# Performance work log

Hardware: AMD Instinct MI355X
Metric: run time of the kernel (lower is better)

The kernel has to match this reference:

```python
import jax, jax.numpy as jnp
import numpy as np

V, E, H, NLAB, NL = 30000, 512, 256, 20, 2
B, T = 32, 512


def setup_inputs() -> dict:
    key = jax.random.key(0)
    ks = jax.random.split(key, 11)
    s = 0.05
    return {
        "input": jax.random.randint(ks[0], (B, T), 0, V, dtype=jnp.int32),
        "mask": jnp.ones((B, T), dtype=bool),
        "embed_table": jax.random.normal(ks[1], (V, E), jnp.float32) * s,
        "Wih": jax.random.normal(ks[2], (NL, 2, 4 * H, E), jnp.float32) * s,  # layer input dim E == 2H
        "Whh": jax.random.normal(ks[3], (NL, 2, 4 * H, H), jnp.float32) * s,
        "bias": jax.random.normal(ks[4], (NL, 2, 4 * H), jnp.float32) * s,  # b_ih + b_hh fused
        "lin_W": jax.random.normal(ks[5], (NLAB, 2 * H), jnp.float32) * s,
        "lin_b": jax.random.normal(ks[6], (NLAB,), jnp.float32) * s,
        "transitions": jax.random.normal(ks[7], (NLAB, NLAB), jnp.float32) * 0.1,
        "start_trans": jax.random.normal(ks[8], (NLAB,), jnp.float32) * 0.1,
        "end_trans": jax.random.normal(ks[9], (NLAB,), jnp.float32) * 0.1,
    }


def _lstm_dir(x, Wih, Whh, b, reverse):
    # x: [B,T,in] -> hs: [B,T,H]
    pre = jnp.swapaxes(x, 0, 1) @ Wih.T + b  # [T,B,4H] input projection precomputed
    h0 = jnp.zeros((x.shape[0], Whh.shape[1]), x.dtype)

    def step(carry, p):
        h, c = carry
        g = p + h @ Whh.T
        i, f, gg, o = jnp.split(g, 4, axis=-1)  # pytorch gate order i,f,g,o
        i = jax.nn.sigmoid(i); f = jax.nn.sigmoid(f)
        gg = jnp.tanh(gg); o = jax.nn.sigmoid(o)
        c = f * c + i * gg
        h = o * jnp.tanh(c)
        return (h, c), h

    _, hs = jax.lax.scan(step, (h0, h0), pre, reverse=reverse)
    return jnp.swapaxes(hs, 0, 1)


def _bilstm(x, Wih, Whh, bias):
    out = x
    for l in range(Wih.shape[0]):
        f = _lstm_dir(out, Wih[l, 0], Whh[l, 0], bias[l, 0], False)
        bwd = _lstm_dir(out, Wih[l, 1], Whh[l, 1], bias[l, 1], True)
        out = jnp.concatenate([f, bwd], axis=-1)
    return out


def _viterbi(em, mask, trans, start, end):
    # em: [B,T,L], mask: [B,T] (mask[:,0] assumed all True, as torchcrf requires)
    Bz, Tz, Lz = em.shape
    ar = jnp.arange(Lz, dtype=jnp.int32)
    score0 = start[None, :] + em[:, 0]

    def step(score, xs):
        em_t, m_t = xs  # [B,L], [B]
        ns = score[:, :, None] + trans[None] + em_t[:, None, :]  # [B,L_prev,L_cur]
        best = ns.max(axis=1)
        idx = ns.argmax(axis=1).astype(jnp.int32)
        score = jnp.where(m_t[:, None], best, score)
        idx = jnp.where(m_t[:, None], idx, ar[None, :])  # identity bp for padded steps
        return score, idx

    em_tb = jnp.swapaxes(em, 0, 1)
    m_tb = jnp.swapaxes(mask, 0, 1)
    score, hist = jax.lax.scan(step, score0, (em_tb[1:], m_tb[1:]))
    score = score + end[None, :]
    last = jnp.argmax(score, axis=-1).astype(jnp.int32)
    bidx = jnp.arange(Bz)

    def back(tag, bp):
        prev = bp[bidx, tag]
        return prev, prev

    _, prevs = jax.lax.scan(back, last, hist, reverse=True)  # prevs[t] = tag_t for t=0..T-2
    tags = jnp.concatenate([prevs, last[None]], axis=0)  # [T,B]
    return jnp.swapaxes(tags, 0, 1), score.max(axis=-1)


def reference(input, mask, embed_table, Wih, Whh, bias, lin_W, lin_b, transitions, start_trans, end_trans):
    x = embed_table[input]                      # [B,T,E]
    h = _bilstm(x, Wih, Whh, bias)              # [B,T,2H]
    em = h @ lin_W.T + lin_b                    # [B,T,L]
    tags, _ = _viterbi(em, mask, transitions, start_trans, end_trans)
    return tags
```

## Files before the change

kernel.cpp:

```cpp
#include <hip/hip_runtime.h>
#include <math.h>


#define T_SEQ   512
#define BATCH   32
#define HID     256
#define NLAB    20

#define AGENT __HIP_MEMORY_SCOPE_AGENT
#define HB_STRIDE 576

__device__ __forceinline__ float fsig(float x) {
  float e = __builtin_amdgcn_exp2f(-1.44269504088896340736f * x);
  return __builtin_amdgcn_rcpf(1.f + e);
}
__device__ __forceinline__ float ftanh(float x) {
  float e = __builtin_amdgcn_exp2f(2.88539008177792681471f * x);
  return 1.f - 2.f * __builtin_amdgcn_rcpf(e + 1.f);
}
__device__ __forceinline__ float addx1(float x) {
  int p = __builtin_amdgcn_update_dpp(0, __float_as_int(x), 0xB1, 0xF, 0xF, true);
  return x + __int_as_float(p);
}
__device__ __forceinline__ float addx2(float x) {
  int p = __builtin_amdgcn_update_dpp(0, __float_as_int(x), 0x4E, 0xF, 0xF, true);
  return x + __int_as_float(p);
}
__device__ __forceinline__ float addx4(float x) {
  int p = __builtin_amdgcn_ds_swizzle(__float_as_int(x), 0x101F);
  return x + __int_as_float(p);
}

__global__ __launch_bounds__(256) void prep_wih_k(const float* __restrict__ Wih,
                                                  const float* __restrict__ bias,
                                                  float* __restrict__ Wp,
                                                  float* __restrict__ bpp) {
  int idx = blockIdx.x * 256 + threadIdx.x;
  int k4 = idx & 127;
  int n  = (idx >> 7) & 1023;
  int ld = idx >> 17;
  int q = n & 3, j = n >> 2;
  int src = ld * 1024 + q * 256 + j;
  ((float4*)Wp)[idx] = ((const float4*)Wih)[(size_t)src * 128 + k4];
  if (k4 == 0) bpp[ld * 1024 + n] = bias[src];
}

__global__ __launch_bounds__(256) void prep_whh_reg_k(const float* __restrict__ Whh,
                                                      float4* __restrict__ Wreg) {
  int idx = blockIdx.x * 256 + threadIdx.x;
  int t  = idx & 511;
  int i  = (idx >> 9) & 31;
  int bx = (idx >> 14) & 3;
  int ld = idx >> 16;
  int u = bx * 64 + (t >> 3);
  int q = i >> 3, c = i & 7;
  int k = (t & 7) * 32 + c * 4;
  Wreg[idx] = ((const float4*)Whh)[((size_t)(ld * 1024 + q * 256 + u) * 256 + k) >> 2];
}

__global__ __launch_bounds__(256) void zero_hbuf_k(int4* __restrict__ p) {
  p[blockIdx.x * 256 + threadIdx.x] = int4{0, 0, 0, 0};
}

__global__ __launch_bounds__(256) void embed_k(const int* __restrict__ inp,
                                               const float* __restrict__ tab,
                                               float* __restrict__ x) {
  int idx = blockIdx.x * 256 + threadIdx.x;
  int row = idx >> 7, c = idx & 127;
  int tok = inp[row];
  ((float4*)x)[idx] = ((const float4*)tab)[(size_t)tok * 128 + c];
}

#define GBM 128
#define GBN 128
#define GBK 32
__global__ __launch_bounds__(256) void gemm_nt_k(const float* __restrict__ A,
                                                 const float* __restrict__ W,
                                                 const float* __restrict__ bias,
                                                 float* __restrict__ C,
                                                 int M, int N, int K) {
  __shared__ float As[GBK][GBM];
  __shared__ float Ws[GBK][GBN];
  int tid = threadIdx.x;
  int bm = blockIdx.x, bn = blockIdx.y;
  int tm = (tid & 15) * 8, tn = (tid >> 4) * 8;
  int r  = tid >> 1;
  int kq = (tid & 1) * 16;
  const float* Ap = A + (size_t)(bm * GBM + r) * K + kq;
  const float* Wq = W + (size_t)(bn * GBN + r) * K + kq;

  float acc[8][8] = {};
  float4 av[4], wv[4];

#pragma unroll
  for (int j = 0; j < 4; ++j) {
    av[j] = *(const float4*)(Ap + 4 * j);
    wv[j] = *(const float4*)(Wq + 4 * j);
  }

  for (int k0 = 0; k0 < K; k0 += GBK) {
    __syncthreads();
#pragma unroll
    for (int j = 0; j < 4; ++j) {
      float ta[4], tw[4];
      *(float4*)ta = av[j]; *(float4*)tw = wv[j];
#pragma unroll
      for (int e = 0; e < 4; ++e) {
        As[kq + 4 * j + e][r] = ta[e];
        Ws[kq + 4 * j + e][r] = tw[e];
      }
    }
    __syncthreads();
    if (k0 + GBK < K) {
#pragma unroll
      for (int j = 0; j < 4; ++j) {
        av[j] = *(const float4*)(Ap + k0 + GBK + 4 * j);
        wv[j] = *(const float4*)(Wq + k0 + GBK + 4 * j);
      }
    }
#pragma unroll
    for (int kk = 0; kk < GBK; ++kk) {
      float a8[8], b8[8];
      *(float4*)&a8[0] = *(const float4*)&As[kk][tm];
      *(float4*)&a8[4] = *(const float4*)&As[kk][tm + 4];
      *(float4*)&b8[0] = *(const float4*)&Ws[kk][tn];
      *(float4*)&b8[4] = *(const float4*)&Ws[kk][tn + 4];
#pragma unroll
      for (int i = 0; i < 8; ++i)
#pragma unroll
        for (int j = 0; j < 8; ++j)
          acc[i][j] = fmaf(a8[i], b8[j], acc[i][j]);
    }
  }

  int m0 = bm * GBM + tm, n0 = bn * GBN + tn;
  float4 bv0 = *(const float4*)(bias + n0);
  float4 bv1 = *(const float4*)(bias + n0 + 4);
#pragma unroll
  for (int i = 0; i < 8; ++i) {
    float4 o0, o1;
    o0.x = acc[i][0] + bv0.x; o0.y = acc[i][1] + bv0.y;
    o0.z = acc[i][2] + bv0.z; o0.w = acc[i][3] + bv0.w;
    o1.x = acc[i][4] + bv1.x; o1.y = acc[i][5] + bv1.y;
    o1.z = acc[i][6] + bv1.z; o1.w = acc[i][7] + bv1.w;
    *(float4*)&C[(size_t)(m0 + i) * N + n0]     = o0;
    *(float4*)&C[(size_t)(m0 + i) * N + n0 + 4] = o1;
  }
}

__global__ __launch_bounds__(512, 1) void lstm_group_k(const float* __restrict__ pre,
                                                       const float4* __restrict__ WregL,
                                                       unsigned long long* __restrict__ hbuf,
                                                       float* __restrict__ Hout) {
  int raw = blockIdx.x;
  int xcd = raw & 7, slot = raw >> 3;
  int g  = xcd * 8 + (slot >> 2);
  int bx = slot & 3;
  int b = g >> 1, d = g & 1;
  int tid = threadIdx.x;
  int kq = tid & 7;
  int uu = tid >> 3;
  int u  = bx * 64 + uu;
  bool lead = (kq == 0);

  __shared__ __align__(16) float hout_s[T_SEQ * 64];
  __shared__ __align__(16) float h_s[2][8 * 36];

  float4 w[32];
  const float4* wp = WregL + ((size_t)(d * 4 + bx) * 32) * 512 + tid;
#pragma unroll
  for (int i = 0; i < 32; ++i) w[i] = wp[i * 512];

  unsigned long long* hb = hbuf + (size_t)g * HB_STRIDE;
  const float* preB = pre + (size_t)b * T_SEQ * 2048 + d * 1024 + bx * 256 + 4 * uu;

  float c = 0.f;

  {
    int t = d ? (T_SEQ - 1) : 0;
    float4 g4 = *(const float4*)(preB + (size_t)t * 2048);
    float iv = fsig(g4.x), fv = fsig(g4.y);
    float zv = ftanh(g4.z), ov = fsig(g4.w);
    c = fv * c + iv * zv;
    float hn = ov * ftanh(c);
    if (lead) {
      unsigned long long pv = (1ULL << 32) | (unsigned long long)__float_as_uint(hn);
      __hip_atomic_store(&hb[256 + u], pv, __ATOMIC_RELAXED, AGENT);
      hout_s[t * 64 + uu] = hn;
    }
  }

  for (int s = 1; s < T_SEQ; ++s) {
    int t = d ? (T_SEQ - 1 - s) : s;
    float4 p4 = *(const float4*)(preB + (size_t)t * 2048);

    if (tid < 256) {
      unsigned long long* hp = &hb[(s & 1) * 256 + tid];
      unsigned long long v;
      for (;;) {
        v = __hip_atomic_load(hp, __ATOMIC_RELAXED, AGENT);
        if (__all((unsigned)(v >> 32) == (unsigned)s)) break;
        __builtin_amdgcn_s_sleep(1);
      }
      h_s[s & 1][(tid >> 5) * 36 + (tid & 31)] = __uint_as_float((unsigned)v);
    }
    __syncthreads();

    const float* hk = &h_s[s & 1][kq * 36];
    float4 a0 = {0.f, 0.f, 0.f, 0.f}, a1 = a0, a2 = a0, a3 = a0;
#pragma unroll
    for (int c8 = 0; c8 < 8; ++c8) {
      float4 h4 = *(const float4*)(hk + 4 * c8);
      a0.x = fmaf(w[c8].x,      h4.x, a0.x); a0.y = fmaf(w[c8].y,      h4.y, a0.y);
      a0.z = fmaf(w[c8].z,      h4.z, a0.z); a0.w = fmaf(w[c8].w,      h4.w, a0.w);
      a1.x = fmaf(w[8 + c8].x,  h4.x, a1.x); a1.y = fmaf(w[8 + c8].y,  h4.y, a1.y);
      a1.z = fmaf(w[8 + c8].z,  h4.z, a1.z); a1.w = fmaf(w[8 + c8].w,  h4.w, a1.w);
      a2.x = fmaf(w[16 + c8].x, h4.x, a2.x); a2.y = fmaf(w[16 + c8].y, h4.y, a2.y);
      a2.z = fmaf(w[16 + c8].z, h4.z, a2.z); a2.w = fmaf(w[16 + c8].w, h4.w, a2.w);
      a3.x = fmaf(w[24 + c8].x, h4.x, a3.x); a3.y = fmaf(w[24 + c8].y, h4.y, a3.y);
      a3.z = fmaf(w[24 + c8].z, h4.z, a3.z); a3.w = fmaf(w[24 + c8].w, h4.w, a3.w);
    }
    float gi = (a0.x + a0.y) + (a0.z + a0.w);
    float gf = (a1.x + a1.y) + (a1.z + a1.w);
    float gg = (a2.x + a2.y) + (a2.z + a2.w);
    float go = (a3.x + a3.y) + (a3.z + a3.w);
    gi = addx4(addx2(addx1(gi))) + p4.x;
    gf = addx4(addx2(addx1(gf))) + p4.y;
    gg = addx4(addx2(addx1(gg))) + p4.z;
    go = addx4(addx2(addx1(go))) + p4.w;

    float iv = fsig(gi), fv = fsig(gf);
    float zv = ftanh(gg), ov = fsig(go);
    c = fv * c + iv * zv;
    float hn = ov * ftanh(c);

    if (lead) {
      if (s < T_SEQ - 1) {
        unsigned long long pv = ((unsigned long long)(unsigned)(s + 1) << 32) |
                                (unsigned long long)__float_as_uint(hn);
        __hip_atomic_store(&hb[((s + 1) & 1) * 256 + u], pv, __ATOMIC_RELAXED, AGENT);
      }
      hout_s[t * 64 + uu] = hn;
    }
  }

  __syncthreads();
  const float4* src = (const float4*)hout_s;
  float4* dst = (float4*)Hout;
#pragma unroll
  for (int i = 0; i < 16; ++i) {
    int idx = i * 512 + tid;
    int t = idx >> 4, c4 = idx & 15;
    dst[((size_t)(b * T_SEQ + t) << 7) + d * 64 + bx * 16 + c4] = src[idx];
  }
}

__global__ __launch_bounds__(256) void linear20_k(const float* __restrict__ H,
                                                  const float* __restrict__ LW,
                                                  const float* __restrict__ lb,
                                                  float* __restrict__ em) {
  __shared__ float hs[8 * 516];
  __shared__ float lws[20 * 516];
  int tid = threadIdx.x;
  int m0 = blockIdx.x * 8;
  const float4* Hp = (const float4*)(H + (size_t)m0 * 512);
  for (int v = tid; v < 1024; v += 256) {
    int rr = v >> 7, cc = v & 127;
    *(float4*)&hs[rr * 516 + cc * 4] = Hp[v];
  }
  for (int v = tid; v < 2560; v += 256) {
    int ll = v >> 7, cc = v & 127;
    *(float4*)&lws[ll * 516 + cc * 4] = ((const float4*)LW)[v];
  }
  __syncthreads();
  if (tid < 160) {
    int rr = tid / 20, ll = tid % 20;
    float acc = 0.f;
    const float* hp = &hs[rr * 516];
    const float* wp = &lws[ll * 516];
#pragma unroll 8
    for (int k = 0; k < 512; ++k) acc += hp[k] * wp[k];
    em[(size_t)(m0 + rr) * 20 + ll] = acc + lb[ll];
  }
}

__global__ __launch_bounds__(640) void viterbi_k(const float* __restrict__ em,
                                                 const float* __restrict__ trans,
                                                 const float* __restrict__ startt,
                                                 const float* __restrict__ endt,
                                                 int* __restrict__ tags) {
  __shared__ float em_s[T_SEQ * NLAB];
  __shared__ float trans_s[NLAB * NLAB];
  __shared__ float score_s[NLAB];
  __shared__ unsigned char bp[(T_SEQ - 1) * NLAB];
  int b = blockIdx.x, tid = threadIdx.x;
  const float4* emb = (const float4*)(em + (size_t)b * T_SEQ * NLAB);
  for (int v = tid; v < T_SEQ * NLAB / 4; v += 640) ((float4*)em_s)[v] = emb[v];
  for (int v = tid; v < NLAB * NLAB; v += 640) trans_s[v] = trans[v];
  if (tid < NLAB) score_s[tid] = startt[tid] + em[(size_t)b * T_SEQ * NLAB + tid];
  __syncthreads();
  int j = tid >> 5;
  int i = tid & 31;
  float tr = (i < NLAB) ? trans_s[i * NLAB + j] : -1e30f;
  for (int t = 1; t < T_SEQ; ++t) {
    float v = (i < NLAB) ? (score_s[i] + tr) : -1e30f;
    int bi = i;
#pragma unroll
    for (int off = 16; off > 0; off >>= 1) {
      float ov = __shfl_down(v, off, 32);
      int oi = __shfl_down(bi, off, 32);
      if (ov > v || (ov == v && oi < bi)) { v = ov; bi = oi; }
    }
    __syncthreads();
    if (i == 0) {
      score_s[j] = v + em_s[t * NLAB + j];
      bp[(t - 1) * NLAB + j] = (unsigned char)bi;
    }
    __syncthreads();
  }
  if (tid == 0) {
    float best = score_s[0] + endt[0]; int cur = 0;
    for (int l = 1; l < NLAB; ++l) {
      float sv = score_s[l] + endt[l];
      if (sv > best) { best = sv; cur = l; }
    }
    int* tb = tags + b * T_SEQ;
    tb[T_SEQ - 1] = cur;
    for (int s2 = T_SEQ - 2; s2 >= 0; --s2) { cur = bp[s2 * NLAB + cur]; tb[s2] = cur; }
  }
}

extern "C" void kernel_launch(void* const* d_in, const int* in_sizes, int n_in,
                              void* d_out, int out_size, void* d_ws, size_t ws_size,
                              hipStream_t stream) {
  const int*   inp   = (const int*)d_in[0];
  const float* tab   = (const float*)d_in[2];
  const float* Wih   = (const float*)d_in[3];
  const float* Whh   = (const float*)d_in[4];
  const float* bias  = (const float*)d_in[5];
  const float* linW  = (const float*)d_in[6];
  const float* linb  = (const float*)d_in[7];
  const float* trans = (const float*)d_in[8];
  const float* stt   = (const float*)d_in[9];
  const float* endt  = (const float*)d_in[10];
  int* tags = (int*)d_out;

  float* ws   = (float*)d_ws;
  float* Wp   = ws;
  float* Wreg = Wp + 2097152;
  float* bpp  = Wreg + 1048576;
  float* x    = bpp + 4096;
  float* H0   = x + 8388608;
  float* pre  = H0 + 8388608;
  float* em   = pre + 33554432;
  unsigned long long* hbuf = (unsigned long long*)em;

  const float4* WregF4 = (const float4*)Wreg;

  hipLaunchKernelGGL(zero_hbuf_k, dim3(144), dim3(256), 0, stream, (int4*)hbuf);
  hipLaunchKernelGGL(prep_wih_k, dim3(2048), dim3(256), 0, stream, Wih, bias, Wp, bpp);
  hipLaunchKernelGGL(prep_whh_reg_k, dim3(1024), dim3(256), 0, stream, Whh, (float4*)Wreg);
  hipLaunchKernelGGL(embed_k, dim3(8192), dim3(256), 0, stream, inp, tab, x);

  const int M = BATCH * T_SEQ;
  hipLaunchKernelGGL(gemm_nt_k, dim3(M / GBM, 2048 / GBN), dim3(256), 0, stream,
                     x, Wp, bpp, pre, M, 2048, 512);
  hipLaunchKernelGGL(lstm_group_k, dim3(256), dim3(512), 0, stream,
                     pre, WregF4, hbuf, H0);
  hipLaunchKernelGGL(gemm_nt_k, dim3(M / GBM, 2048 / GBN), dim3(256), 0, stream,
                     H0, Wp + 2048 * 512, bpp + 2048, pre, M, 2048, 512);
  hipLaunchKernelGGL(lstm_group_k, dim3(256), dim3(512), 0, stream,
                     pre, WregF4 + 2 * 65536, hbuf + 64 * HB_STRIDE, x);
  hipLaunchKernelGGL(linear20_k, dim3(M / 8), dim3(256), 0, stream, x, linW, linb, em);
  hipLaunchKernelGGL(viterbi_k, dim3(BATCH), dim3(640), 0, stream, em, trans, stt, endt, tags);
}
```

Baseline: 2.990 ms.

## Add XCD-local L2 fast path for LSTM hidden-state exchange, DPP row reduction

Each LSTM step now publishes the hidden-state word twice: a plain store to a new buffer, read back with an sc0 inline-asm load so it hits the XCD-local L2, and the old agent-scope atomic store. Readers poll the L2-coherent copy up to six times before falling back to the agent-scope spin loop. The point is to cut the latency of cross-block synchronisation inside one XCD group, since the blocks of a group are mapped onto the same XCD. The ds_swizzle in the lane reduction is also replaced with a DPP row_shr/row-half move, and the zeroed sync region is doubled. This relies on undocumented cache behaviour and on the blocks being co-located. Each step now issues extra stores and polls, and the fallback adds latency whenever the fast path misses.

```diff
diff --git a/kernel.cpp b/kernel.cpp
--- a/kernel.cpp
+++ b/kernel.cpp
@@ -9,6 +9,7 @@
 
 #define AGENT __HIP_MEMORY_SCOPE_AGENT
 #define HB_STRIDE 576
+#define HB_LAYER  (64 * HB_STRIDE)
 
 __device__ __forceinline__ float fsig(float x) {
   float e = __builtin_amdgcn_exp2f(-1.44269504088896340736f * x);
@@ -26,9 +27,19 @@
   int p = __builtin_amdgcn_update_dpp(0, __float_as_int(x), 0x4E, 0xF, 0xF, true);
   return x + __int_as_float(p);
 }
-__device__ __forceinline__ float addx4(float x) {
-  int p = __builtin_amdgcn_ds_swizzle(__float_as_int(x), 0x101F);
+__device__ __forceinline__ float addx4h(float x) {
+  int p = __builtin_amdgcn_update_dpp(0, __float_as_int(x), 0x141, 0xF, 0xF, true);
   return x + __int_as_float(p);
+}
+
+__device__ __forceinline__ void store_l2(unsigned long long* p, unsigned long long v) {
+  asm volatile("global_store_dwordx2 %0, %1, off" :: "v"(p), "v"(v) : "memory");
+}
+__device__ __forceinline__ unsigned long long load_l2(const unsigned long long* p) {
+  unsigned long long v;
+  asm volatile("global_load_dwordx2 %0, %1, off sc0\n\ts_waitcnt vmcnt(0)"
+               : "=v"(v) : "v"(p) : "memory");
+  return v;
 }
 
 __global__ __launch_bounds__(256) void prep_wih_k(const float* __restrict__ Wih,
@@ -150,7 +161,8 @@
 
 __global__ __launch_bounds__(512, 1) void lstm_group_k(const float* __restrict__ pre,
                                                        const float4* __restrict__ WregL,
-                                                       unsigned long long* __restrict__ hbuf,
+                                                       unsigned long long* __restrict__ hbufA,
+                                                       unsigned long long* __restrict__ hbufB,
                                                        float* __restrict__ Hout) {
   int raw = blockIdx.x;
   int xcd = raw & 7, slot = raw >> 3;
@@ -171,7 +183,8 @@
 #pragma unroll
   for (int i = 0; i < 32; ++i) w[i] = wp[i * 512];
 
-  unsigned long long* hb = hbuf + (size_t)g * HB_STRIDE;
+  unsigned long long* hbA = hbufA + (size_t)g * HB_STRIDE;
+  unsigned long long* hbB = hbufB + (size_t)g * HB_STRIDE;
   const float* preB = pre + (size_t)b * T_SEQ * 2048 + d * 1024 + bx * 256 + 4 * uu;
 
   float c = 0.f;
@@ -185,7 +198,8 @@
     float hn = ov * ftanh(c);
     if (lead) {
       unsigned long long pv = (1ULL << 32) | (unsigned long long)__float_as_uint(hn);
-      __hip_atomic_store(&hb[256 + u], pv, __ATOMIC_RELAXED, AGENT);
+      store_l2(&hbA[256 + u], pv);
+      __hip_atomic_store(&hbB[256 + u], pv, __ATOMIC_RELAXED, AGENT);
       hout_s[t * 64 + uu] = hn;
     }
   }
@@ -195,12 +209,20 @@
     float4 p4 = *(const float4*)(preB + (size_t)t * 2048);
 
     if (tid < 256) {
-      unsigned long long* hp = &hb[(s & 1) * 256 + tid];
+      unsigned long long* pa = &hbA[(s & 1) * 256 + tid];
+      unsigned long long* pb = &hbB[(s & 1) * 256 + tid];
       unsigned long long v;
-      for (;;) {
-        v = __hip_atomic_load(hp, __ATOMIC_RELAXED, AGENT);
-        if (__all((unsigned)(v >> 32) == (unsigned)s)) break;
-        __builtin_amdgcn_s_sleep(1);
+      bool got = false;
+      for (int tries = 0; tries < 6; ++tries) {
+        v = load_l2(pa);
+        if (__all((unsigned)(v >> 32) == (unsigned)s)) { got = true; break; }
+      }
+      if (!got) {
+        for (;;) {
+          v = __hip_atomic_load(pb, __ATOMIC_RELAXED, AGENT);
+          if (__all((unsigned)(v >> 32) == (unsigned)s)) break;
+          __builtin_amdgcn_s_sleep(1);
+        }
       }
       h_s[s & 1][(tid >> 5) * 36 + (tid & 31)] = __uint_as_float((unsigned)v);
     }
@@ -224,10 +246,10 @@
     float gf = (a1.x + a1.y) + (a1.z + a1.w);
     float gg = (a2.x + a2.y) + (a2.z + a2.w);
     float go = (a3.x + a3.y) + (a3.z + a3.w);
-    gi = addx4(addx2(addx1(gi))) + p4.x;
-    gf = addx4(addx2(addx1(gf))) + p4.y;
-    gg = addx4(addx2(addx1(gg))) + p4.z;
-    go = addx4(addx2(addx1(go))) + p4.w;
+    gi = addx4h(addx2(addx1(gi))) + p4.x;
+    gf = addx4h(addx2(addx1(gf))) + p4.y;
+    gg = addx4h(addx2(addx1(gg))) + p4.z;
+    go = addx4h(addx2(addx1(go))) + p4.w;
 
     float iv = fsig(gi), fv = fsig(gf);
     float zv = ftanh(gg), ov = fsig(go);
@@ -238,7 +260,8 @@
       if (s < T_SEQ - 1) {
         unsigned long long pv = ((unsigned long long)(unsigned)(s + 1) << 32) |
                                 (unsigned long long)__float_as_uint(hn);
-        __hip_atomic_store(&hb[((s + 1) & 1) * 256 + u], pv, __ATOMIC_RELAXED, AGENT);
+        store_l2(&hbA[((s + 1) & 1) * 256 + u], pv);
+        __hip_atomic_store(&hbB[((s + 1) & 1) * 256 + u], pv, __ATOMIC_RELAXED, AGENT);
       }
       hout_s[t * 64 + uu] = hn;
     }
@@ -353,11 +376,12 @@
   float* H0   = x + 8388608;
   float* pre  = H0 + 8388608;
   float* em   = pre + 33554432;
-  unsigned long long* hbuf = (unsigned long long*)em;
+  unsigned long long* hbufA = (unsigned long long*)em;
+  unsigned long long* hbufB = hbufA + 2 * HB_LAYER;
 
   const float4* WregF4 = (const float4*)Wreg;
 
-  hipLaunchKernelGGL(zero_hbuf_k, dim3(144), dim3(256), 0, stream, (int4*)hbuf);
+  hipLaunchKernelGGL(zero_hbuf_k, dim3(288), dim3(256), 0, stream, (int4*)hbufA);
   hipLaunchKernelGGL(prep_wih_k, dim3(2048), dim3(256), 0, stream, Wih, bias, Wp, bpp);
   hipLaunchKernelGGL(prep_whh_reg_k, dim3(1024), dim3(256), 0, stream, Whh, (float4*)Wreg);
   hipLaunchKernelGGL(embed_k, dim3(8192), dim3(256), 0, stream, inp, tab, x);
@@ -366,11 +390,11 @@
   hipLaunchKernelGGL(gemm_nt_k, dim3(M / GBM, 2048 / GBN), dim3(256), 0, stream,
                      x, Wp, bpp, pre, M, 2048, 512);
   hipLaunchKernelGGL(lstm_group_k, dim3(256), dim3(512), 0, stream,
-                     pre, WregF4, hbuf, H0);
+                     pre, WregF4, hbufA, hbufB, H0);
   hipLaunchKernelGGL(gemm_nt_k, dim3(M / GBM, 2048 / GBN), dim3(256), 0, stream,
                      H0, Wp + 2048 * 512, bpp + 2048, pre, M, 2048, 512);
   hipLaunchKernelGGL(lstm_group_k, dim3(256), dim3(512), 0, stream,
-                     pre, WregF4 + 2 * 65536, hbuf + 64 * HB_STRIDE, x);
+                     pre, WregF4 + 2 * 65536, hbufA + HB_LAYER, hbufB + HB_LAYER, x);
   hipLaunchKernelGGL(linear20_k, dim3(M / 8), dim3(256), 0, stream, x, linW, linb, em);
   hipLaunchKernelGGL(viterbi_k, dim3(BATCH), dim3(640), 0, stream, em, trans, stt, endt, tags);
 }
```

After: 2.844 ms. 4.9% less time.
